# Performance work log

Measured on AMD Instinct MI355X. Metric: run time of the kernel, lower is better.

Reference implementation:

```python
import jax, jax.numpy as jnp
import numpy as np

D = 2048
N_SLOTS = 8
ALPHA_MIN = 0.02
FAST_DECAY = 0.95
ALPHA_BOOST = 1.0
B = 16384


def setup_inputs() -> dict:
    key = jax.random.key(0)
    ks = jax.random.split(key, 12)
    h = jax.random.normal(ks[0], (B, D), dtype=jnp.float32)
    neighbor_msg = jax.random.normal(ks[1], (B, D), dtype=jnp.float32)
    keys = jax.random.normal(ks[2], (N_SLOTS, D), dtype=jnp.float32) / (D ** 0.5)
    # torch nn.Linear convention: W [out, in], y = x @ W.T + b
    Wr = jax.random.normal(ks[3], (D, D), dtype=jnp.float32) * 0.02
    br = jnp.zeros((D,), dtype=jnp.float32)
    Wc = jax.random.normal(ks[4], (2, 2 * D), dtype=jnp.float32) * 0.02
    bc = jnp.zeros((2,), dtype=jnp.float32)
    Ww = jax.random.normal(ks[5], (D, 2 * D), dtype=jnp.float32) * 0.02
    bw = jnp.zeros((D,), dtype=jnp.float32)
    state = jax.random.normal(ks[6], (N_SLOTS, D), dtype=jnp.float32) * 0.1
    fast = jax.random.normal(ks[7], (N_SLOTS, D), dtype=jnp.float32) * 0.1
    return {"h": h, "neighbor_msg": neighbor_msg, "keys": keys,
            "Wr": Wr, "br": br, "Wc": Wc, "bc": bc, "Ww": Ww, "bw": bw,
            "state": state, "fast": fast}


def reference(h, neighbor_msg, keys, Wr, br, Wc, bc, Ww, bw, state, fast):
    # read_proj
    q = h @ Wr.T + br                                  # [B, D]
    attn = jax.nn.softmax(q @ keys.T, axis=-1)         # [B, n_slots]
    read = attn @ (state + fast)                       # [B, D]
    # ctrl -> add/erase gates (erase computed but unused downstream, as in source)
    ctrl = jnp.concatenate([h, read], axis=-1) @ Wc.T + bc   # [B, 2]
    add = jax.nn.sigmoid(ctrl[:, 0:1])
    erase = jax.nn.sigmoid(ctrl[:, 1:2])
    alpha = jnp.clip(ALPHA_MIN + (1.0 - ALPHA_MIN) * jnp.mean(add), 0.0, 1.0)
    alpha = jnp.clip(alpha * ALPHA_BOOST, 0.0, 1.0)
    # attention-weighted write into slots
    w_in = jnp.concatenate([h + neighbor_msg, read], axis=-1)  # [B, 2D]
    delta = attn.T @ (w_in @ Ww.T + bw)                # [n_slots, D]
    new_state = (1.0 - alpha) * state + alpha * delta
    new_fast = FAST_DECAY * fast + (1.0 - FAST_DECAY) * delta
    return read, attn, alpha, new_state, new_fast
```

## Files before the change

### kernel.cpp

```cpp
#include <hip/hip_runtime.h>
#include <math.h>

#define D 2048
#define NS 8
#define BTOT 16384

#define ATTN_OFF  ((size_t)BTOT * D)
#define ALPHA_OFF (ATTN_OFF + (size_t)BTOT * NS)
#define STATE_OFF (ALPHA_OFF + 1)
#define FAST_OFF  (STATE_OFF + (size_t)NS * D)

#define WS_SM    0
#define WS_KP    16384
#define WS_KPP   32768
#define WS_GS    294912
#define WS_P     311296
#define WS_HWC   327680
#define WS_LB    344064
#define WS_SWC   344072
#define WS_G     344080
#define WS_ALPHA 344153
#define WS_PPART 344160

static __device__ __forceinline__ float4 f4fma(float s, float4 a, float4 c) {
  c.x += s * a.x; c.y += s * a.y; c.z += s * a.z; c.w += s * a.w; return c;
}

__global__ void kZ(const float* __restrict__ st, const float* __restrict__ fa,
                   float* __restrict__ sm, float* __restrict__ gall) {
  int i = blockIdx.x * 256 + threadIdx.x;
  sm[i] = st[i] + fa[i];
  if (blockIdx.x == 0 && threadIdx.x < 73) gall[threadIdx.x] = 0.f;
}

__global__ void __launch_bounds__(256) kA(const float* __restrict__ keys,
                                          const float* __restrict__ Wr,
                                          float* __restrict__ kpp) {
  int ec = blockIdx.x, dc = blockIdx.y, t = threadIdx.x;
  int e = ec * 256 + t;
  float acc[NS] = {0.f,0.f,0.f,0.f,0.f,0.f,0.f,0.f};
  int d0 = dc * 128;
  for (int d = d0; d < d0 + 128; ++d) {
    float wv = Wr[(size_t)d * D + e];
#pragma unroll
    for (int s = 0; s < NS; ++s) acc[s] += keys[s * D + d] * wv;
  }
#pragma unroll
  for (int s = 0; s < NS; ++s) kpp[(size_t)(dc * NS + s) * D + e] = acc[s];
}

__global__ void kB(const float* __restrict__ kpp, float* __restrict__ kp) {
  int i = blockIdx.x * 256 + threadIdx.x;
  float sum = 0.f;
#pragma unroll
  for (int dc = 0; dc < 16; ++dc) sum += kpp[dc * 16384 + i];
  kp[i] = sum;
}

__global__ void __launch_bounds__(256) kC(const float* __restrict__ keys,
                                          const float* __restrict__ br,
                                          const float* __restrict__ Wc,
                                          const float* __restrict__ sm,
                                          float* __restrict__ lb, float* __restrict__ swc) {
  int t = threadIdx.x;
  float aL[NS] = {0.f,0.f,0.f,0.f,0.f,0.f,0.f,0.f};
  float aS[NS] = {0.f,0.f,0.f,0.f,0.f,0.f,0.f,0.f};
  for (int idx = t; idx < D; idx += 256) {
    float brv = br[idx];
    float wcr = Wc[D + idx];
#pragma unroll
    for (int s = 0; s < NS; ++s) {
      aL[s] += keys[s * D + idx] * brv;
      aS[s] += sm[s * D + idx] * wcr;
    }
  }
#pragma unroll
  for (int off = 32; off > 0; off >>= 1) {
#pragma unroll
    for (int s = 0; s < NS; ++s) {
      aL[s] += __shfl_down(aL[s], off);
      aS[s] += __shfl_down(aS[s], off);
    }
  }
  __shared__ float red[4 * 16];
  int lane = t & 63, wid = t >> 6;
  if (lane == 0) {
#pragma unroll
    for (int s = 0; s < NS; ++s) { red[wid * 16 + s] = aL[s]; red[wid * 16 + 8 + s] = aS[s]; }
  }
  __syncthreads();
  if (t < 16) {
    float v = red[t] + red[16 + t] + red[32 + t] + red[48 + t];
    if (t < 8) lb[t] = v; else swc[t - 8] = v;
  }
}

__global__ void __launch_bounds__(256) k1(const float* __restrict__ h, const float* __restrict__ Wc,
                                          const float* __restrict__ kp, const float* __restrict__ lb,
                                          float* __restrict__ attn, float* __restrict__ hwc) {
  int b = blockIdx.x, t = threadIdx.x;
  const float4* hr = (const float4*)(h + (size_t)b * D);
  float4 ha = hr[t], hb = hr[t + 256];
  float acc[9];
  const float4* kp4 = (const float4*)kp;
#pragma unroll
  for (int s = 0; s < NS; ++s) {
    float4 ka = kp4[s * 512 + t], kb = kp4[s * 512 + 256 + t];
    acc[s] = ha.x * ka.x + ha.y * ka.y + ha.z * ka.z + ha.w * ka.w
           + hb.x * kb.x + hb.y * kb.y + hb.z * kb.z + hb.w * kb.w;
  }
  {
    const float4* wc4 = (const float4*)Wc;
    float4 wa = wc4[t], wb = wc4[256 + t];
    acc[8] = ha.x * wa.x + ha.y * wa.y + ha.z * wa.z + ha.w * wa.w
           + hb.x * wb.x + hb.y * wb.y + hb.z * wb.z + hb.w * wb.w;
  }
#pragma unroll
  for (int off = 32; off > 0; off >>= 1) {
#pragma unroll
    for (int v = 0; v < 9; ++v) acc[v] += __shfl_down(acc[v], off);
  }
  __shared__ float red[36];
  int lane = t & 63, wid = t >> 6;
  if (lane == 0) {
#pragma unroll
    for (int v = 0; v < 9; ++v) red[wid * 9 + v] = acc[v];
  }
  __syncthreads();
  if (t == 0) {
    float l[9];
#pragma unroll
    for (int v = 0; v < 9; ++v) l[v] = red[v] + red[9 + v] + red[18 + v] + red[27 + v];
    float lg[8]; float m = -1e30f;
#pragma unroll
    for (int s = 0; s < NS; ++s) { lg[s] = l[s] + lb[s]; m = fmaxf(m, lg[s]); }
    float ex[8]; float sum = 0.f;
#pragma unroll
    for (int s = 0; s < NS; ++s) { ex[s] = expf(lg[s] - m); sum += ex[s]; }
    float inv = 1.f / sum;
    float* ao = attn + (size_t)b * NS;
#pragma unroll
    for (int s = 0; s < NS; ++s) ao[s] = ex[s] * inv;
    hwc[b] = l[8];
  }
}

__global__ void __launch_bounds__(256) k2(const float* __restrict__ h, const float* __restrict__ nm,
                                          const float* __restrict__ sm, const float* __restrict__ attn,
                                          float* __restrict__ readout, float* __restrict__ ppart,
                                          int rows_per) {
  int t = threadIdx.x;
  int hsel = blockIdx.x & 1, rc = blockIdx.x >> 1;
  int fi = hsel * 256 + t;
  const float4* sm4 = (const float4*)sm;
  float4 S[NS];
#pragma unroll
  for (int s = 0; s < NS; ++s) S[s] = sm4[s * 512 + fi];
  float4 P[NS];
#pragma unroll
  for (int s = 0; s < NS; ++s) P[s] = make_float4(0.f, 0.f, 0.f, 0.f);
  int b0 = rc * rows_per;
  for (int r = 0; r < rows_per; ++r) {
    int b = b0 + r;
    float4 hv = ((const float4*)(h + (size_t)b * D))[fi];
    float4 nv = ((const float4*)(nm + (size_t)b * D))[fi];
    const float4* ar = (const float4*)(attn + (size_t)b * NS);
    float4 a0 = ar[0], a1 = ar[1];
    float av[NS] = {a0.x, a0.y, a0.z, a0.w, a1.x, a1.y, a1.z, a1.w};
    float4 w = make_float4(hv.x + nv.x, hv.y + nv.y, hv.z + nv.z, hv.w + nv.w);
    float4 rd = make_float4(0.f, 0.f, 0.f, 0.f);
#pragma unroll
    for (int s = 0; s < NS; ++s) {
      rd = f4fma(av[s], S[s], rd);
      P[s] = f4fma(av[s], w, P[s]);
    }
    ((float4*)(readout + (size_t)b * D))[fi] = rd;
  }
  float4* pp = (float4*)(ppart + (size_t)blockIdx.x * NS * 1024);
#pragma unroll
  for (int s = 0; s < NS; ++s) pp[s * 256 + t] = P[s];
}

__global__ void __launch_bounds__(256) k2b(const float* __restrict__ attn, const float* __restrict__ hwc,
                                           const float* __restrict__ swc, const float* __restrict__ bc,
                                           float* __restrict__ gall) {
  int t = threadIdx.x;
  int b = blockIdx.x * 256 + t;
  const float4* ar = (const float4*)(attn + (size_t)b * NS);
  float4 a0 = ar[0], a1 = ar[1];
  float av[NS] = {a0.x, a0.y, a0.z, a0.w, a1.x, a1.y, a1.z, a1.w};
  float x = hwc[b] + bc[0];
#pragma unroll
  for (int s = 0; s < NS; ++s) x += av[s] * swc[s];
  float add = 1.f / (1.f + expf(-x));
  float v[73];
#pragma unroll
  for (int i = 0; i < NS; ++i)
#pragma unroll
    for (int j = 0; j < NS; ++j) v[i * 8 + j] = av[i] * av[j];
#pragma unroll
  for (int s = 0; s < NS; ++s) v[64 + s] = av[s];
  v[72] = add;
#pragma unroll
  for (int off = 32; off > 0; off >>= 1) {
#pragma unroll
    for (int k = 0; k < 73; ++k) v[k] += __shfl_down(v[k], off);
  }
  __shared__ float red[4 * 73];
  int lane = t & 63, wid = t >> 6;
  if (lane == 0) {
#pragma unroll
    for (int k = 0; k < 73; ++k) red[wid * 73 + k] = v[k];
  }
  __syncthreads();
  if (t < 73) {
    float tot = red[t] + red[73 + t] + red[146 + t] + red[219 + t];
    atomicAdd(&gall[t], tot);
  }
}

__global__ void k3(const float* __restrict__ ppart, const float* __restrict__ gall,
                   const float* __restrict__ sm, float* __restrict__ p, float* __restrict__ gs,
                   float* __restrict__ alphap, float* __restrict__ alphaout, int NC) {
  int tid = blockIdx.x * 256 + threadIdx.x;
  if (tid < 16384) {
    int s = tid >> 11, e = tid & 2047;
    int hsel = e >> 10, ec = e & 1023;
    float sum = 0.f;
    for (int rc = 0; rc < NC; ++rc)
      sum += ppart[((size_t)(rc * 2 + hsel) * NS + s) * 1024 + ec];
    p[tid] = sum;
  } else {
    int i = tid - 16384;
    int s = i >> 11, e = i & 2047;
    float sum = 0.f;
#pragma unroll
    for (int sp = 0; sp < NS; ++sp) sum += gall[s * 8 + sp] * sm[sp * D + e];
    gs[i] = sum;
  }
  if (tid == 0) {
    float mean = gall[72] * (1.f / (float)BTOT);
    float al = 0.02f + 0.98f * mean;
    al = fminf(fmaxf(al, 0.f), 1.f);
    alphap[0] = al;
    alphaout[0] = al;
  }
}

__global__ void __launch_bounds__(256) k4(const float* __restrict__ Ww, const float* __restrict__ bw,
                                          const float* __restrict__ st, const float* __restrict__ fa,
                                          const float* __restrict__ p, const float* __restrict__ gs,
                                          const float* __restrict__ cs, const float* __restrict__ alphap,
                                          float* __restrict__ outst, float* __restrict__ outfa) {
  int dd = blockIdx.x, t = threadIdx.x;
  const float4* wr = (const float4*)(Ww + (size_t)dd * (2 * D));
  float4 w0 = wr[t], w1 = wr[256 + t], w2 = wr[512 + t], w3 = wr[768 + t];
  const float4* p4 = (const float4*)p;
  const float4* g4 = (const float4*)gs;
  float acc[NS];
#pragma unroll
  for (int s = 0; s < NS; ++s) {
    float4 pa = p4[s * 512 + t], pb = p4[s * 512 + 256 + t];
    float4 ga = g4[s * 512 + t], gb = g4[s * 512 + 256 + t];
    acc[s] = w0.x * pa.x + w0.y * pa.y + w0.z * pa.z + w0.w * pa.w
           + w1.x * pb.x + w1.y * pb.y + w1.z * pb.z + w1.w * pb.w
           + w2.x * ga.x + w2.y * ga.y + w2.z * ga.z + w2.w * ga.w
           + w3.x * gb.x + w3.y * gb.y + w3.z * gb.z + w3.w * gb.w;
  }
#pragma unroll
  for (int off = 32; off > 0; off >>= 1) {
#pragma unroll
    for (int v = 0; v < NS; ++v) acc[v] += __shfl_down(acc[v], off);
  }
  __shared__ float red[32];
  int lane = t & 63, wid = t >> 6;
  if (lane == 0) {
#pragma unroll
    for (int v = 0; v < NS; ++v) red[wid * 8 + v] = acc[v];
  }
  __syncthreads();
  if (t < NS) {
    float tot = red[t] + red[8 + t] + red[16 + t] + red[24 + t];
    float delta = tot + cs[t] * bw[dd];
    float al = alphap[0];
    size_t idx = (size_t)t * D + dd;
    outst[idx] = (1.f - al) * st[idx] + al * delta;
    outfa[idx] = 0.95f * fa[idx] + 0.05f * delta;
  }
}

extern "C" void kernel_launch(void* const* d_in, const int* in_sizes, int n_in,
                              void* d_out, int out_size, void* d_ws, size_t ws_size,
                              hipStream_t stream) {
  const float* h    = (const float*)d_in[0];
  const float* nm   = (const float*)d_in[1];
  const float* keys = (const float*)d_in[2];
  const float* Wr   = (const float*)d_in[3];
  const float* br   = (const float*)d_in[4];
  const float* Wc   = (const float*)d_in[5];
  const float* bc   = (const float*)d_in[6];
  const float* Ww   = (const float*)d_in[7];
  const float* bw   = (const float*)d_in[8];
  const float* st   = (const float*)d_in[9];
  const float* fa   = (const float*)d_in[10];
  float* out = (float*)d_out;
  float* ws  = (float*)d_ws;

  size_t ws_floats = ws_size / 4;
  int NC = 0;
  for (int c = 256; c >= 1; c >>= 1) {
    if ((size_t)WS_PPART + (size_t)c * 16384 <= ws_floats) { NC = c; break; }
  }
  if (NC == 0) NC = 1;
  int rows_per = BTOT / NC;

  float* sm   = ws + WS_SM;
  float* kp   = ws + WS_KP;
  float* kpp  = ws + WS_KPP;
  float* gsb  = ws + WS_GS;
  float* pb   = ws + WS_P;
  float* hwc  = ws + WS_HWC;
  float* lb   = ws + WS_LB;
  float* swc  = ws + WS_SWC;
  float* gall = ws + WS_G;
  float* alphap = ws + WS_ALPHA;
  float* ppart  = ws + WS_PPART;
  float* attn   = out + ATTN_OFF;

  kZ<<<64, 256, 0, stream>>>(st, fa, sm, gall);
  kA<<<dim3(8, 16), 256, 0, stream>>>(keys, Wr, kpp);
  kB<<<64, 256, 0, stream>>>(kpp, kp);
  kC<<<1, 256, 0, stream>>>(keys, br, Wc, sm, lb, swc);
  k1<<<BTOT, 256, 0, stream>>>(h, Wc, kp, lb, attn, hwc);
  k2<<<2 * NC, 256, 0, stream>>>(h, nm, sm, attn, out, ppart, rows_per);
  k2b<<<64, 256, 0, stream>>>(attn, hwc, swc, bc, gall);
  k3<<<128, 256, 0, stream>>>(ppart, gall, sm, pb, gsb, alphap, out + ALPHA_OFF, NC);
  k4<<<2048, 256, 0, stream>>>(Ww, bw, st, fa, pb, gsb, ws + WS_G + 64, alphap, out + STATE_OFF, out + FAST_OFF);
}
```

Baseline: 553.9 us.

## Restructure logits and read/write passes with tiled blocks and atomic reductions

Replaces the per-row logit kernel (one block per batch row) with a tiled kernel in which each wave handles 64 rows by a 256-column chunk. It stages h through LDS and accumulates 9 logits per row with atomics. Softmax and the gate are moved into a separate small kernel. The read/write-partial pass now uses a 2D grid whose partials are reduced in LDS and then atomically added into the slot buffer, and the kp partial-sum kernel becomes atomics. This removes the ppart workspace and the reduction kernels, at the cost of many float atomics and nondeterministic summation order.

```diff
diff --git a/kernel.cpp b/kernel.cpp
--- a/kernel.cpp
+++ b/kernel.cpp
@@ -11,50 +11,46 @@
 #define FAST_OFF  (STATE_OFF + (size_t)NS * D)
 
 #define WS_SM    0
-#define WS_KP    16384
-#define WS_KPP   32768
-#define WS_GS    294912
-#define WS_P     311296
-#define WS_HWC   327680
-#define WS_LB    344064
-#define WS_SWC   344072
-#define WS_G     344080
-#define WS_ALPHA 344153
-#define WS_PPART 344160
-
-static __device__ __forceinline__ float4 f4fma(float s, float4 a, float4 c) {
-  c.x += s * a.x; c.y += s * a.y; c.z += s * a.z; c.w += s * a.w; return c;
-}
-
-__global__ void kZ(const float* __restrict__ st, const float* __restrict__ fa,
-                   float* __restrict__ sm, float* __restrict__ gall) {
+#define WS_KPX   16384
+#define WS_GS    34816
+#define WS_PB    51200
+#define WS_LOG   67584
+#define WS_LB    215040
+#define WS_SWC   215048
+#define WS_GALL  215056
+#define WS_ALPHA 215136
+
+__global__ void __launch_bounds__(256) kZ(const float* __restrict__ st, const float* __restrict__ fa,
+                                          const float* __restrict__ Wc, float* __restrict__ ws) {
   int i = blockIdx.x * 256 + threadIdx.x;
-  sm[i] = st[i] + fa[i];
-  if (blockIdx.x == 0 && threadIdx.x < 73) gall[threadIdx.x] = 0.f;
+  if (i < 16384) {
+    ws[WS_SM + i] = st[i] + fa[i];
+  } else if (i < 32768) {
+    ws[WS_KPX + (i - 16384)] = 0.f;
+  } else if (i < 34816) {
+    ws[WS_KPX + 16384 + (i - 32768)] = Wc[i - 32768];
+  } else if (i < 51200) {
+    ws[WS_PB + (i - 34816)] = 0.f;
+  } else if (i < 198656) {
+    ws[WS_LOG + (i - 51200)] = 0.f;
+  } else if (i < 198736) {
+    ws[WS_GALL + (i - 198656)] = 0.f;
+  }
 }
 
 __global__ void __launch_bounds__(256) kA(const float* __restrict__ keys,
                                           const float* __restrict__ Wr,
-                                          float* __restrict__ kpp) {
-  int ec = blockIdx.x, dc = blockIdx.y, t = threadIdx.x;
-  int e = ec * 256 + t;
+                                          float* __restrict__ kpx) {
+  int e = blockIdx.x * 256 + threadIdx.x;
+  int d0 = blockIdx.y * 128;
   float acc[NS] = {0.f,0.f,0.f,0.f,0.f,0.f,0.f,0.f};
-  int d0 = dc * 128;
   for (int d = d0; d < d0 + 128; ++d) {
     float wv = Wr[(size_t)d * D + e];
 #pragma unroll
     for (int s = 0; s < NS; ++s) acc[s] += keys[s * D + d] * wv;
   }
 #pragma unroll
-  for (int s = 0; s < NS; ++s) kpp[(size_t)(dc * NS + s) * D + e] = acc[s];
-}
-
-__global__ void kB(const float* __restrict__ kpp, float* __restrict__ kp) {
-  int i = blockIdx.x * 256 + threadIdx.x;
-  float sum = 0.f;
-#pragma unroll
-  for (int dc = 0; dc < 16; ++dc) sum += kpp[dc * 16384 + i];
-  kp[i] = sum;
+  for (int s = 0; s < NS; ++s) atomicAdd(&kpx[s * D + e], acc[s]);
 }
 
 __global__ void __launch_bounds__(256) kC(const float* __restrict__ keys,
@@ -95,101 +91,61 @@
   }
 }
 
-__global__ void __launch_bounds__(256) k1(const float* __restrict__ h, const float* __restrict__ Wc,
-                                          const float* __restrict__ kp, const float* __restrict__ lb,
-                                          float* __restrict__ attn, float* __restrict__ hwc) {
-  int b = blockIdx.x, t = threadIdx.x;
-  const float4* hr = (const float4*)(h + (size_t)b * D);
-  float4 ha = hr[t], hb = hr[t + 256];
-  float acc[9];
-  const float4* kp4 = (const float4*)kp;
-#pragma unroll
-  for (int s = 0; s < NS; ++s) {
-    float4 ka = kp4[s * 512 + t], kb = kp4[s * 512 + 256 + t];
-    acc[s] = ha.x * ka.x + ha.y * ka.y + ha.z * ka.z + ha.w * ka.w
-           + hb.x * kb.x + hb.y * kb.y + hb.z * kb.z + hb.w * kb.w;
-  }
-  {
-    const float4* wc4 = (const float4*)Wc;
-    float4 wa = wc4[t], wb = wc4[256 + t];
-    acc[8] = ha.x * wa.x + ha.y * wa.y + ha.z * wa.z + ha.w * wa.w
-           + hb.x * wb.x + hb.y * wb.y + hb.z * wb.z + hb.w * wb.w;
-  }
-#pragma unroll
-  for (int off = 32; off > 0; off >>= 1) {
-#pragma unroll
-    for (int v = 0; v < 9; ++v) acc[v] += __shfl_down(acc[v], off);
-  }
-  __shared__ float red[36];
-  int lane = t & 63, wid = t >> 6;
-  if (lane == 0) {
-#pragma unroll
-    for (int v = 0; v < 9; ++v) red[wid * 9 + v] = acc[v];
-  }
-  __syncthreads();
-  if (t == 0) {
-    float l[9];
-#pragma unroll
-    for (int v = 0; v < 9; ++v) l[v] = red[v] + red[9 + v] + red[18 + v] + red[27 + v];
-    float lg[8]; float m = -1e30f;
-#pragma unroll
-    for (int s = 0; s < NS; ++s) { lg[s] = l[s] + lb[s]; m = fmaxf(m, lg[s]); }
-    float ex[8]; float sum = 0.f;
-#pragma unroll
-    for (int s = 0; s < NS; ++s) { ex[s] = expf(lg[s] - m); sum += ex[s]; }
-    float inv = 1.f / sum;
-    float* ao = attn + (size_t)b * NS;
-#pragma unroll
-    for (int s = 0; s < NS; ++s) ao[s] = ex[s] * inv;
-    hwc[b] = l[8];
-  }
-}
-
-__global__ void __launch_bounds__(256) k2(const float* __restrict__ h, const float* __restrict__ nm,
-                                          const float* __restrict__ sm, const float* __restrict__ attn,
-                                          float* __restrict__ readout, float* __restrict__ ppart,
-                                          int rows_per) {
+__global__ void __launch_bounds__(256) k1a(const float* __restrict__ h,
+                                           const float* __restrict__ kpx,
+                                           float* __restrict__ logits) {
+  __shared__ float lds[4][64 * 65];
   int t = threadIdx.x;
-  int hsel = blockIdx.x & 1, rc = blockIdx.x >> 1;
-  int fi = hsel * 256 + t;
-  const float4* sm4 = (const float4*)sm;
-  float4 S[NS];
-#pragma unroll
-  for (int s = 0; s < NS; ++s) S[s] = sm4[s * 512 + fi];
-  float4 P[NS];
-#pragma unroll
-  for (int s = 0; s < NS; ++s) P[s] = make_float4(0.f, 0.f, 0.f, 0.f);
-  int b0 = rc * rows_per;
-  for (int r = 0; r < rows_per; ++r) {
-    int b = b0 + r;
-    float4 hv = ((const float4*)(h + (size_t)b * D))[fi];
-    float4 nv = ((const float4*)(nm + (size_t)b * D))[fi];
-    const float4* ar = (const float4*)(attn + (size_t)b * NS);
-    float4 a0 = ar[0], a1 = ar[1];
-    float av[NS] = {a0.x, a0.y, a0.z, a0.w, a1.x, a1.y, a1.z, a1.w};
-    float4 w = make_float4(hv.x + nv.x, hv.y + nv.y, hv.z + nv.z, hv.w + nv.w);
-    float4 rd = make_float4(0.f, 0.f, 0.f, 0.f);
-#pragma unroll
-    for (int s = 0; s < NS; ++s) {
-      rd = f4fma(av[s], S[s], rd);
-      P[s] = f4fma(av[s], w, P[s]);
-    }
-    ((float4*)(readout + (size_t)b * D))[fi] = rd;
-  }
-  float4* pp = (float4*)(ppart + (size_t)blockIdx.x * NS * 1024);
-#pragma unroll
-  for (int s = 0; s < NS; ++s) pp[s * 256 + t] = P[s];
-}
-
-__global__ void __launch_bounds__(256) k2b(const float* __restrict__ attn, const float* __restrict__ hwc,
-                                           const float* __restrict__ swc, const float* __restrict__ bc,
-                                           float* __restrict__ gall) {
+  int w = t >> 6, lane = t & 63;
+  int wave_id = blockIdx.x * 4 + w;
+  int rg = wave_id >> 3, chunk = wave_id & 7;
+  int rowbase = rg * 64, colbase = chunk * 256;
+  float acc[9] = {0.f,0.f,0.f,0.f,0.f,0.f,0.f,0.f,0.f};
+  int c16 = lane & 15, rq = lane >> 4;
+  for (int sub = 0; sub < 4; ++sub) {
+    int cb = colbase + sub * 64;
+#pragma unroll
+    for (int i = 0; i < 16; ++i) {
+      int r = i * 4 + rq;
+      float4 v = *(const float4*)(h + (size_t)(rowbase + r) * D + cb + c16 * 4);
+      float* dst = &lds[w][r * 65 + c16 * 4];
+      dst[0] = v.x; dst[1] = v.y; dst[2] = v.z; dst[3] = v.w;
+    }
+    __syncthreads();
+    const float* hr = &lds[w][lane * 65];
+#pragma unroll
+    for (int j4 = 0; j4 < 16; ++j4) {
+      float h0 = hr[j4 * 4 + 0], h1 = hr[j4 * 4 + 1], h2 = hr[j4 * 4 + 2], h3 = hr[j4 * 4 + 3];
+#pragma unroll
+      for (int s = 0; s < 9; ++s) {
+        const float* kr = kpx + s * D + cb + j4 * 4;
+        acc[s] += h0 * kr[0] + h1 * kr[1] + h2 * kr[2] + h3 * kr[3];
+      }
+    }
+    __syncthreads();
+  }
+#pragma unroll
+  for (int s = 0; s < 9; ++s) atomicAdd(&logits[(size_t)(rowbase + lane) * 9 + s], acc[s]);
+}
+
+__global__ void __launch_bounds__(256) k1b(const float* __restrict__ logits,
+                                           const float* __restrict__ lb, const float* __restrict__ swc,
+                                           const float* __restrict__ bc,
+                                           float* __restrict__ attn, float* __restrict__ gall) {
   int t = threadIdx.x;
   int b = blockIdx.x * 256 + t;
-  const float4* ar = (const float4*)(attn + (size_t)b * NS);
-  float4 a0 = ar[0], a1 = ar[1];
-  float av[NS] = {a0.x, a0.y, a0.z, a0.w, a1.x, a1.y, a1.z, a1.w};
-  float x = hwc[b] + bc[0];
+  const float* lrow = logits + (size_t)b * 9;
+  float lg[NS]; float m = -1e30f;
+#pragma unroll
+  for (int s = 0; s < NS; ++s) { lg[s] = lrow[s] + lb[s]; m = fmaxf(m, lg[s]); }
+  float av[NS]; float sum = 0.f;
+#pragma unroll
+  for (int s = 0; s < NS; ++s) { av[s] = expf(lg[s] - m); sum += av[s]; }
+  float inv = 1.f / sum;
+  float* ao = attn + (size_t)b * NS;
+#pragma unroll
+  for (int s = 0; s < NS; ++s) { av[s] *= inv; ao[s] = av[s]; }
+  float x = lrow[8] + bc[0];
 #pragma unroll
   for (int s = 0; s < NS; ++s) x += av[s] * swc[s];
   float add = 1.f / (1.f + expf(-x));
@@ -219,26 +175,64 @@
   }
 }
 
-__global__ void k3(const float* __restrict__ ppart, const float* __restrict__ gall,
-                   const float* __restrict__ sm, float* __restrict__ p, float* __restrict__ gs,
-                   float* __restrict__ alphap, float* __restrict__ alphaout, int NC) {
-  int tid = blockIdx.x * 256 + threadIdx.x;
-  if (tid < 16384) {
-    int s = tid >> 11, e = tid & 2047;
-    int hsel = e >> 10, ec = e & 1023;
-    float sum = 0.f;
-    for (int rc = 0; rc < NC; ++rc)
-      sum += ppart[((size_t)(rc * 2 + hsel) * NS + s) * 1024 + ec];
-    p[tid] = sum;
-  } else {
-    int i = tid - 16384;
-    int s = i >> 11, e = i & 2047;
-    float sum = 0.f;
-#pragma unroll
-    for (int sp = 0; sp < NS; ++sp) sum += gall[s * 8 + sp] * sm[sp * D + e];
-    gs[i] = sum;
-  }
-  if (tid == 0) {
+static __device__ __forceinline__ float4 f4fma(float s, float4 a, float4 c) {
+  c.x += s * a.x; c.y += s * a.y; c.z += s * a.z; c.w += s * a.w; return c;
+}
+
+__global__ void __launch_bounds__(256) k2n(const float* __restrict__ h, const float* __restrict__ nm,
+                                           const float* __restrict__ sm, const float* __restrict__ attn,
+                                           float* __restrict__ readout, float* __restrict__ pb) {
+  __shared__ float4 lp[4][NS][64];
+  int t = threadIdx.x;
+  int c4 = t & 63, r4 = t >> 6;
+  int chunk = blockIdx.x, rc = blockIdx.y;
+  int fbase = chunk * 64 + c4;
+  const float4* sm4 = (const float4*)sm;
+  float4 S[NS];
+#pragma unroll
+  for (int s = 0; s < NS; ++s) S[s] = sm4[s * 512 + fbase];
+  float4 P[NS];
+#pragma unroll
+  for (int s = 0; s < NS; ++s) P[s] = make_float4(0.f, 0.f, 0.f, 0.f);
+  int rowbase = rc * 256;
+  for (int it = 0; it < 64; ++it) {
+    int row = rowbase + it * 4 + r4;
+    float4 hv = ((const float4*)h)[(size_t)row * 512 + fbase];
+    float4 nv = ((const float4*)nm)[(size_t)row * 512 + fbase];
+    const float* ar = attn + (size_t)row * NS;
+    float4 w = make_float4(hv.x + nv.x, hv.y + nv.y, hv.z + nv.z, hv.w + nv.w);
+    float4 rd = make_float4(0.f, 0.f, 0.f, 0.f);
+#pragma unroll
+    for (int s = 0; s < NS; ++s) {
+      float a = ar[s];
+      rd = f4fma(a, S[s], rd);
+      P[s] = f4fma(a, w, P[s]);
+    }
+    ((float4*)readout)[(size_t)row * 512 + fbase] = rd;
+  }
+#pragma unroll
+  for (int s = 0; s < NS; ++s) lp[r4][s][c4] = P[s];
+  __syncthreads();
+  for (int k = t; k < 512; k += 256) {
+    int s = k >> 6, c = k & 63;
+    float4 a = lp[0][s][c], b = lp[1][s][c], cc = lp[2][s][c], d = lp[3][s][c];
+    float4 v = make_float4(a.x + b.x + cc.x + d.x, a.y + b.y + cc.y + d.y,
+                           a.z + b.z + cc.z + d.z, a.w + b.w + cc.w + d.w);
+    float* dst = pb + s * D + chunk * 256 + c * 4;
+    atomicAdd(dst + 0, v.x); atomicAdd(dst + 1, v.y);
+    atomicAdd(dst + 2, v.z); atomicAdd(dst + 3, v.w);
+  }
+}
+
+__global__ void k3n(const float* __restrict__ gall, const float* __restrict__ sm,
+                    float* __restrict__ gs, float* __restrict__ alphap, float* __restrict__ alphaout) {
+  int i = blockIdx.x * 256 + threadIdx.x;
+  int s = i >> 11, e = i & 2047;
+  float sum = 0.f;
+#pragma unroll
+  for (int sp = 0; sp < NS; ++sp) sum += gall[s * 8 + sp] * sm[sp * D + e];
+  gs[i] = sum;
+  if (i == 0) {
     float mean = gall[72] * (1.f / (float)BTOT);
     float al = 0.02f + 0.98f * mean;
     al = fminf(fmaxf(al, 0.f), 1.f);
@@ -260,10 +254,10 @@
   float acc[NS];
 #pragma unroll
   for (int s = 0; s < NS; ++s) {
-    float4 pa = p4[s * 512 + t], pb = p4[s * 512 + 256 + t];
+    float4 pa = p4[s * 512 + t], pb2 = p4[s * 512 + 256 + t];
     float4 ga = g4[s * 512 + t], gb = g4[s * 512 + 256 + t];
     acc[s] = w0.x * pa.x + w0.y * pa.y + w0.z * pa.z + w0.w * pa.w
-           + w1.x * pb.x + w1.y * pb.y + w1.z * pb.z + w1.w * pb.w
+           + w1.x * pb2.x + w1.y * pb2.y + w1.z * pb2.z + w1.w * pb2.w
            + w2.x * ga.x + w2.y * ga.y + w2.z * ga.z + w2.w * ga.w
            + w3.x * gb.x + w3.y * gb.y + w3.z * gb.z + w3.w * gb.w;
   }
@@ -306,34 +300,23 @@
   float* out = (float*)d_out;
   float* ws  = (float*)d_ws;
 
-  size_t ws_floats = ws_size / 4;
-  int NC = 0;
-  for (int c = 256; c >= 1; c >>= 1) {
-    if ((size_t)WS_PPART + (size_t)c * 16384 <= ws_floats) { NC = c; break; }
-  }
-  if (NC == 0) NC = 1;
-  int rows_per = BTOT / NC;
-
-  float* sm   = ws + WS_SM;
-  float* kp   = ws + WS_KP;
-  float* kpp  = ws + WS_KPP;
-  float* gsb  = ws + WS_GS;
-  float* pb   = ws + WS_P;
-  float* hwc  = ws + WS_HWC;
-  float* lb   = ws + WS_LB;
-  float* swc  = ws + WS_SWC;
-  float* gall = ws + WS_G;
+  float* sm     = ws + WS_SM;
+  float* kpx    = ws + WS_KPX;
+  float* gsb    = ws + WS_GS;
+  float* pb     = ws + WS_PB;
+  float* logits = ws + WS_LOG;
+  float* lb     = ws + WS_LB;
+  float* swc    = ws + WS_SWC;
+  float* gall   = ws + WS_GALL;
   float* alphap = ws + WS_ALPHA;
-  float* ppart  = ws + WS_PPART;
   float* attn   = out + ATTN_OFF;
 
-  kZ<<<64, 256, 0, stream>>>(st, fa, sm, gall);
-  kA<<<dim3(8, 16), 256, 0, stream>>>(keys, Wr, kpp);
-  kB<<<64, 256, 0, stream>>>(kpp, kp);
+  kZ<<<777, 256, 0, stream>>>(st, fa, Wc, ws);
+  kA<<<dim3(8, 16), 256, 0, stream>>>(keys, Wr, kpx);
   kC<<<1, 256, 0, stream>>>(keys, br, Wc, sm, lb, swc);
-  k1<<<BTOT, 256, 0, stream>>>(h, Wc, kp, lb, attn, hwc);
-  k2<<<2 * NC, 256, 0, stream>>>(h, nm, sm, attn, out, ppart, rows_per);
-  k2b<<<64, 256, 0, stream>>>(attn, hwc, swc, bc, gall);
-  k3<<<128, 256, 0, stream>>>(ppart, gall, sm, pb, gsb, alphap, out + ALPHA_OFF, NC);
-  k4<<<2048, 256, 0, stream>>>(Ww, bw, st, fa, pb, gsb, ws + WS_G + 64, alphap, out + STATE_OFF, out + FAST_OFF);
-}
+  k1a<<<512, 256, 0, stream>>>(h, kpx, logits);
+  k1b<<<64, 256, 0, stream>>>(logits, lb, swc, bc, attn, gall);
+  k2n<<<dim3(8, 64), 256, 0, stream>>>(h, nm, sm, attn, out, pb);
+  k3n<<<64, 256, 0, stream>>>(gall, sm, gsb, alphap, out + ALPHA_OFF);
+  k4<<<2048, 256, 0, stream>>>(Ww, bw, st, fa, pb, gsb, gall + 64, alphap, out + STATE_OFF, out + FAST_OFF);
+}
```

After: 493.9 us. -10.8%, faster.
